# Kernel tuning notes

Hardware: AMD Instinct MI355X
Metric: run time of the kernel (lower is better)

## Reference

```python
import jax, jax.numpy as jnp
import numpy as np

N_NODES = 10000
W_DIM = 512
N_EDGES = 200000


def setup_inputs() -> dict:
    key = jax.random.key(0)
    k1, k2, k3 = jax.random.split(key, 3)
    z_drug = jax.random.normal(k1, (N_NODES, W_DIM), dtype=jnp.float32)
    # glorot-style init for the bilinear weight
    glorot_std = jnp.sqrt(2.0 / (W_DIM + W_DIM)).astype(jnp.float32)
    weight = jax.random.normal(k2, (W_DIM, W_DIM), dtype=jnp.float32) * glorot_std
    batch_edges = jax.random.randint(k3, (2, N_EDGES), 0, N_NODES, dtype=jnp.int64)
    return {"z_drug": z_drug, "weight": weight, "batch_edges": batch_edges}


def reference(z_drug, weight, batch_edges):
    # edge_type == 'drug_drug': both endpoints come from the drug table.
    row_embed = z_drug[batch_edges[0]]  # [E, d]
    col_embed = z_drug[batch_edges[1]]  # [E, d]
    # score_e = row_e @ W @ col_e  == diag((Z1 W) Z2^T) without the N x N blowup
    score = jnp.einsum('ed,df,ef->e', row_embed, weight, col_embed)
    return jax.nn.sigmoid(score)  # is_sigmoid=True default
```

## Files before the change

kernel.cpp:

```cpp
#include <hip/hip_runtime.h>
#include <math.h>

#define DIM     512
#define NNODES  10000
#define NEDGES  200000
#define MPAD    10240
#define NMB     160
#define NGRP    5
#define NB      (NGRP * NNODES)
#define SCAN_N  49
#define GEMM_GRID (NMB * 4)

#define SCAT_BASE  49
#define SCAT_N     196
#define GEMM_BASE  245
#define FUSE_GRID  (GEMM_BASE + GEMM_GRID)

using floatx4 = __attribute__((ext_vector_type(4))) float;
using half8   = __attribute__((ext_vector_type(8))) _Float16;
using half2v  = __attribute__((ext_vector_type(2))) _Float16;
typedef unsigned long long ull;

template <int N> struct IC { static constexpr int v = N; };

__device__ inline float dot2acc(half2v a, half2v b, float c) {
#if __has_builtin(__builtin_amdgcn_fdot2)
    return __builtin_amdgcn_fdot2(a, b, c, false);
#else
    return fmaf((float)a[0], (float)b[0], fmaf((float)a[1], (float)b[1], c));
#endif
}

__device__ inline int aload(const int* p) {
    return __hip_atomic_load(p, __ATOMIC_RELAXED, __HIP_MEMORY_SCOPE_AGENT);
}
__device__ inline void astore(int* p, int v) {
    __hip_atomic_store(p, v, __ATOMIC_RELAXED, __HIP_MEMORY_SCOPE_AGENT);
}
__device__ inline void waitflag(int* f, int target) {
    while (__hip_atomic_load(f, __ATOMIC_RELAXED, __HIP_MEMORY_SCOPE_AGENT) < target)
        __builtin_amdgcn_s_sleep(8);
    __atomic_signal_fence(__ATOMIC_ACQUIRE);
}
__device__ inline void signal(int* f) {
    __atomic_signal_fence(__ATOMIC_RELEASE);
    __hip_atomic_fetch_add(f, 1, __ATOMIC_RELAXED, __HIP_MEMORY_SCOPE_AGENT);
}

#define PREP_ZBLK 2560
#define PREP_WBASE PREP_ZBLK
#define PREP_HBASE (PREP_ZBLK + 64)
#define PREP_HBLK  64
#define PREP_GRID  (PREP_HBASE + PREP_HBLK)
__global__ __launch_bounds__(256) void prep(const float* __restrict__ Z,
                                            const float* __restrict__ W,
                                            const int* __restrict__ eidx,
                                            _Float16* __restrict__ Zh16,
                                            _Float16* __restrict__ Wh16t,
                                            int* __restrict__ counts) {
    const int b = blockIdx.x;
    const int t = threadIdx.x;

    if (b < PREP_ZBLK) {
        const int idx8 = (b * 256 + t) * 8;
        const int m = idx8 >> 9;
        float x[8];
        if (m < NNODES) {
            float4 v0 = *(const float4*)(Z + idx8);
            float4 v1 = *(const float4*)(Z + idx8 + 4);
            x[0]=v0.x; x[1]=v0.y; x[2]=v0.z; x[3]=v0.w;
            x[4]=v1.x; x[5]=v1.y; x[6]=v1.z; x[7]=v1.w;
        } else {
            #pragma unroll
            for (int j = 0; j < 8; ++j) x[j] = 0.f;
        }
        half8 h;
        #pragma unroll
        for (int j = 0; j < 8; ++j) h[j] = (_Float16)x[j];
        *(half8*)(Zh16 + idx8) = h;
    } else if (b < PREP_HBASE) {
        __shared__ float tile[64][65];
        const int wb = b - PREP_WBASE;
        const int kb = (wb >> 3) * 64;
        const int nb = (wb & 7) * 64;
        const int kk = t >> 2;
        const int ch = t & 3;

        const float* src = W + (size_t)(kb + kk) * DIM + nb + ch * 16;
        #pragma unroll
        for (int q = 0; q < 4; ++q) {
            float4 v = *(const float4*)(src + q * 4);
            tile[kk][ch * 16 + q * 4 + 0] = v.x;
            tile[kk][ch * 16 + q * 4 + 1] = v.y;
            tile[kk][ch * 16 + q * 4 + 2] = v.z;
            tile[kk][ch * 16 + q * 4 + 3] = v.w;
        }
        __syncthreads();

        const int nn = kk;
        half8 h0, h1;
        #pragma unroll
        for (int i = 0; i < 8; ++i) h0[i] = (_Float16)tile[ch * 16 + i][nn];
        #pragma unroll
        for (int i = 0; i < 8; ++i) h1[i] = (_Float16)tile[ch * 16 + 8 + i][nn];
        _Float16* d = Wh16t + (size_t)(nb + nn) * DIM + kb + ch * 16;
        *(half8*)(d)     = h0;
        *(half8*)(d + 8) = h1;
    } else {
        const int hb = b - PREP_HBASE;
        for (int e = hb * 256 + t; e < NEDGES; e += PREP_HBLK * 256) {
            int r = eidx[e];
            int c = eidx[NEDGES + e];
            atomicAdd(&counts[(c >> 11) * NNODES + r], 1);
        }
    }
}

__global__ __launch_bounds__(256, 3) void gemm_sort(
        const _Float16* __restrict__ Zh16,
        const _Float16* __restrict__ Wh16t,
        _Float16* __restrict__ ZWh,
        const int* __restrict__ eidx,
        int* __restrict__ counts,
        int* __restrict__ cursor,
        int* __restrict__ blksum,
        ull* __restrict__ slots,
        int* __restrict__ flags)
{
    __shared__ _Float16 Abuf[2][2 * 64 * 32];
    __shared__ _Float16 Bbuf[2][2 * 128 * 32];
    __shared__ int wsum[4];
    __shared__ int sbase;

    const int t   = threadIdx.x;
    const int bid = blockIdx.x;

    if (bid >= GEMM_BASE) {
        const int s8  = bid - GEMM_BASE;
        const int cxd = bid & 7;
        const int rr  = s8 >> 3;
        const int mg  = (rr >> 2) * 8 + cxd;
        const int m0  = mg * 64;
        const int n0  = (rr & 3) * 128;

        const int l  = t & 63;
        const int w  = t >> 6;
        const int wn = w * 32;
        const int lm = l & 15;
        const int lq = l >> 4;
        const unsigned wbase = (unsigned)(t & 192);

        floatx4 acc[4][2] = {};

        auto stage = [&](int buf, int k0) {
            #pragma unroll
            for (int p = 0; p < 2; ++p) {
                const int s   = p * 256 + t;
                const int kk  = s >> 8;
                const int row = (s >> 2) & 63;
                const int ch  = s & 3;
                const _Float16* src = Zh16 + (size_t)(m0 + row) * DIM + k0 + kk * 32 + ch * 8;
                __builtin_amdgcn_global_load_lds(
                    (const __attribute__((address_space(1))) void*)src,
                    (__attribute__((address_space(3))) void*)&Abuf[buf][(p * 256 + wbase) * 8],
                    16, 0, 0);
            }
            #pragma unroll
            for (int p = 0; p < 4; ++p) {
                const int s   = p * 256 + t;
                const int kk  = s >> 9;
                const int row = (s >> 2) & 127;
                const int ch  = s & 3;
                const _Float16* src = Wh16t + (size_t)(n0 + row) * DIM + k0 + kk * 32 + ch * 8;
                __builtin_amdgcn_global_load_lds(
                    (const __attribute__((address_space(1))) void*)src,
                    (__attribute__((address_space(3))) void*)&Bbuf[buf][(p * 256 + wbase) * 8],
                    16, 0, 0);
            }
        };

        stage(0, 0);
        stage(1, 64);

        auto step = [&](auto Sc) {
            constexpr int S   = decltype(Sc)::v;
            constexpr int buf = S & 1;
            if constexpr (S < 7) asm volatile("s_waitcnt vmcnt(6)" ::: "memory");
            else                 asm volatile("s_waitcnt vmcnt(0)" ::: "memory");
            __builtin_amdgcn_sched_barrier(0);
            __builtin_amdgcn_s_barrier();
            __builtin_amdgcn_sched_barrier(0);

            half8 aF[2][4], bF[2][2];
            #pragma unroll
            for (int kk = 0; kk < 2; ++kk) {
                #pragma unroll
                for (int i = 0; i < 4; ++i)
                    aF[kk][i] = *(const half8*)&Abuf[buf][kk * 2048 + (16 * i + lm) * 32 + lq * 8];
                #pragma unroll
                for (int j = 0; j < 2; ++j)
                    bF[kk][j] = *(const half8*)&Bbuf[buf][kk * 4096 + (wn + 16 * j + lm) * 32 + lq * 8];
            }
            asm volatile("s_waitcnt lgkmcnt(0)" ::: "memory");
            __builtin_amdgcn_sched_barrier(0);
            __builtin_amdgcn_s_barrier();
            __builtin_amdgcn_sched_barrier(0);

            if constexpr (S < 6) stage(buf, (S + 2) * 64);

            #pragma unroll
            for (int kk = 0; kk < 2; ++kk)
                #pragma unroll
                for (int i = 0; i < 4; ++i)
                    #pragma unroll
                    for (int j = 0; j < 2; ++j)
                        acc[i][j] = __builtin_amdgcn_mfma_f32_16x16x32_f16(
                            aF[kk][i], bF[kk][j], acc[i][j], 0, 0, 0);
        };

        step(IC<0>{}); step(IC<1>{}); step(IC<2>{}); step(IC<3>{});
        step(IC<4>{}); step(IC<5>{}); step(IC<6>{}); step(IC<7>{});

        #pragma unroll
        for (int i = 0; i < 4; ++i)
            #pragma unroll
            for (int j = 0; j < 2; ++j)
                #pragma unroll
                for (int r = 0; r < 4; ++r) {
                    const int gm = m0 + 16 * i + lq * 4 + r;
                    const int gn = n0 + wn + 16 * j + lm;
                    if (gm < NNODES)
                        ZWh[(size_t)gm * DIM + gn] = (_Float16)acc[i][j][r];
                }
        return;
    }

    if (bid < SCAT_BASE) {
        const int b = bid;
        const int lane = t & 63;
        const int wv   = t >> 6;

        const int base = b * 1024 + t * 4;
        int v0 = 0, v1 = 0, v2 = 0, v3 = 0;
        if (base + 3 < NB) {
            v0 = aload(counts + base);
            v1 = aload(counts + base + 1);
            v2 = aload(counts + base + 2);
            v3 = aload(counts + base + 3);
        } else {
            if (base     < NB) v0 = aload(counts + base);
            if (base + 1 < NB) v1 = aload(counts + base + 1);
            if (base + 2 < NB) v2 = aload(counts + base + 2);
        }
        const int ts = v0 + v1 + v2 + v3;
        int incl = ts;
        #pragma unroll
        for (int off = 1; off < 64; off <<= 1) {
            int u = __shfl_up(incl, off, 64);
            if (lane >= off) incl += u;
        }
        if (lane == 63) wsum[wv] = incl;
        __syncthreads();
        int wb = 0;
        #pragma unroll
        for (int k = 0; k < 4; ++k) if (k < wv) wb += wsum[k];
        const int ex   = wb + incl - ts;
        const int pre0 = ex;
        const int pre1 = ex + v0;
        const int pre2 = pre1 + v1;
        const int pre3 = pre2 + v2;
        if (t == 255) astore(blksum + b, wb + incl);
        __syncthreads();
        if (t == 0) { signal(&flags[1]); waitflag(&flags[1], SCAN_N); }
        __syncthreads();

        if (t < 64) {
            int v = (t < b) ? aload(blksum + t) : 0;
            #pragma unroll
            for (int off = 32; off > 0; off >>= 1)
                v += __shfl_xor(v, off, 64);
            if (t == 0) sbase = v;
        }
        __syncthreads();
        const int b0 = sbase;

        if (base + 3 < NB) {
            astore(cursor + base,     b0 + pre0);
            astore(cursor + base + 1, b0 + pre1);
            astore(cursor + base + 2, b0 + pre2);
            astore(cursor + base + 3, b0 + pre3);
        } else {
            if (base     < NB) astore(cursor + base,     b0 + pre0);
            if (base + 1 < NB) astore(cursor + base + 1, b0 + pre1);
            if (base + 2 < NB) astore(cursor + base + 2, b0 + pre2);
        }
        __syncthreads();
        if (t == 0) signal(&flags[2]);
        return;
    }

    {
        if (t == 0) waitflag(&flags[2], SCAN_N);
        __syncthreads();

        for (int e = (bid - SCAT_BASE) * 256 + t; e < NEDGES; e += SCAT_N * 256) {
            int r = eidx[e];
            int c = eidx[NEDGES + e];
            int pos = atomicAdd(&cursor[(c >> 11) * NNODES + r], 1);
            slots[pos] = (ull)(((unsigned)c << 18) | (unsigned)e) | ((ull)(unsigned)r << 32);
        }
    }
}

__global__ __launch_bounds__(256) void edge_score_f(const _Float16* __restrict__ ZWh,
                                                    const _Float16* __restrict__ Zh,
                                                    const ull* __restrict__ slots,
                                                    float* __restrict__ out) {
    const int t    = threadIdx.x;
    const int wgid = blockIdx.x * 4 + (t >> 6);
    const int lane = t & 63;
    const int gq   = lane >> 4;
    const int sl   = lane & 15;

    const int ii = wgid * 4 + gq;
    const ull  v = slots[ii];
    const unsigned k = (unsigned)v;
    const int c = (int)(k >> 18);
    const int r = (int)((v >> 32) & 0xFFFFu);

    const _Float16* rp = ZWh + (size_t)r * DIM + sl * 32;
    const _Float16* cp = Zh  + (size_t)c * DIM + sl * 32;

    half8 ra0 = *(const half8*)(rp);
    half8 ra1 = *(const half8*)(rp + 8);
    half8 ra2 = *(const half8*)(rp + 16);
    half8 ra3 = *(const half8*)(rp + 24);
    half8 c0  = *(const half8*)(cp);
    half8 c1  = *(const half8*)(cp + 8);
    half8 c2  = *(const half8*)(cp + 16);
    half8 c3  = *(const half8*)(cp + 24);

    float s = 0.f;
    #pragma unroll
    for (int d = 0; d < 4; ++d) {
        s = dot2acc((half2v){ra0[2*d], ra0[2*d+1]}, (half2v){c0[2*d], c0[2*d+1]}, s);
        s = dot2acc((half2v){ra1[2*d], ra1[2*d+1]}, (half2v){c1[2*d], c1[2*d+1]}, s);
        s = dot2acc((half2v){ra2[2*d], ra2[2*d+1]}, (half2v){c2[2*d], c2[2*d+1]}, s);
        s = dot2acc((half2v){ra3[2*d], ra3[2*d+1]}, (half2v){c3[2*d], c3[2*d+1]}, s);
    }

    s += __shfl_xor(s, 1, 64);
    s += __shfl_xor(s, 2, 64);
    s += __shfl_xor(s, 4, 64);
    s += __shfl_xor(s, 8, 64);

    if (sl == 0)
        out[k & 0x3FFFFu] = 1.0f / (1.0f + expf(-s));
}

#define GTM 128
#define GTN 64
#define GTK 16
#define LDA 132
#define LDB 68

__global__ __launch_bounds__(256) void gemm_zw(const float* __restrict__ A,
                                               const float* __restrict__ B,
                                               float* __restrict__ C) {
    __shared__ float As[GTK * LDA];
    __shared__ float Bs[GTK * LDB];

    const int t  = threadIdx.x;
    const int m0 = blockIdx.x * GTM;
    const int n0 = blockIdx.y * GTN;
    const int tx = t & 15;
    const int ty = t >> 4;

    float acc[8][4] = {};

    for (int k0 = 0; k0 < DIM; k0 += GTK) {
        #pragma unroll
        for (int p = 0; p < 2; ++p) {
            int f  = t + p * 256;
            int mm = f >> 2;
            int kq = f & 3;
            int m  = m0 + mm;
            float4 v = make_float4(0.f, 0.f, 0.f, 0.f);
            if (m < NNODES)
                v = *(const float4*)(A + (size_t)m * DIM + k0 + kq * 4);
            As[(kq * 4 + 0) * LDA + mm] = v.x;
            As[(kq * 4 + 1) * LDA + mm] = v.y;
            As[(kq * 4 + 2) * LDA + mm] = v.z;
            As[(kq * 4 + 3) * LDA + mm] = v.w;
        }
        {
            int kb = t >> 4, n4 = t & 15;
            *(float4*)&Bs[kb * LDB + n4 * 4] =
                *(const float4*)(B + (size_t)(k0 + kb) * DIM + n0 + n4 * 4);
        }
        __syncthreads();

        #pragma unroll
        for (int kk = 0; kk < GTK; ++kk) {
            float4 a0 = *(const float4*)&As[kk * LDA + ty * 8];
            float4 a1 = *(const float4*)&As[kk * LDA + ty * 8 + 4];
            float4 b  = *(const float4*)&Bs[kk * LDB + tx * 4];
            float av[8] = {a0.x, a0.y, a0.z, a0.w, a1.x, a1.y, a1.z, a1.w};
            float bv[4] = {b.x, b.y, b.z, b.w};
            #pragma unroll
            for (int i = 0; i < 8; ++i)
                #pragma unroll
                for (int j = 0; j < 4; ++j)
                    acc[i][j] = fmaf(av[i], bv[j], acc[i][j]);
        }
        __syncthreads();
    }

    #pragma unroll
    for (int i = 0; i < 8; ++i) {
        int m = m0 + ty * 8 + i;
        if (m < NNODES)
            *(float4*)(C + (size_t)m * DIM + n0 + tx * 4) =
                make_float4(acc[i][0], acc[i][1], acc[i][2], acc[i][3]);
    }
}

__global__ __launch_bounds__(256) void edge_score(const float* __restrict__ ZW,
                                                  const float* __restrict__ Z,
                                                  const int* __restrict__ eidx,
                                                  float* __restrict__ out) {
    const int e    = blockIdx.x * 4 + (threadIdx.x >> 6);
    const int lane = threadIdx.x & 63;

    const int r = eidx[e];
    const int c = eidx[NEDGES + e];

    const float4* pr = (const float4*)(ZW + (size_t)r * DIM);
    const float4* pc = (const float4*)(Z  + (size_t)c * DIM);

    float4 a0 = pr[lane * 2 + 0];
    float4 a1 = pr[lane * 2 + 1];
    float4 b0 = pc[lane * 2 + 0];
    float4 b1 = pc[lane * 2 + 1];

    float s = a0.x * b0.x;
    s = fmaf(a0.y, b0.y, s);
    s = fmaf(a0.z, b0.z, s);
    s = fmaf(a0.w, b0.w, s);
    s = fmaf(a1.x, b1.x, s);
    s = fmaf(a1.y, b1.y, s);
    s = fmaf(a1.z, b1.z, s);
    s = fmaf(a1.w, b1.w, s);

    #pragma unroll
    for (int off = 32; off > 0; off >>= 1)
        s += __shfl_xor(s, off, 64);

    if (lane == 0)
        out[e] = 1.0f / (1.0f + expf(-s));
}

extern "C" void kernel_launch(void* const* d_in, const int* in_sizes, int n_in,
                              void* d_out, int out_size, void* d_ws, size_t ws_size,
                              hipStream_t stream) {
    const float* Z  = (const float*)d_in[0];
    const float* W  = (const float*)d_in[1];
    const int*   EI = (const int*)d_in[2];
    float* out = (float*)d_out;

    char* p = (char*)d_ws;
    _Float16* ZWh   = (_Float16*)p;  p += (size_t)MPAD * DIM * 2;
    _Float16* Zh16  = (_Float16*)p;  p += (size_t)MPAD * DIM * 2;
    _Float16* Wh16t = (_Float16*)p;  p += (size_t)DIM * DIM * 2;
    int* counts  = (int*)p;          p += (size_t)NB * 4;
    int* flags   = (int*)p;          p += 4 * 4;
    int* cursor  = (int*)p;          p += (size_t)NB * 4;
    int* blksum  = (int*)p;          p += (size_t)SCAN_N * 4;
    ull* slots   = (ull*)p;          p += (size_t)NEDGES * 8;
    const size_t need_full = (size_t)(p - (char*)d_ws);

    if (ws_size >= need_full) {
        hipMemsetAsync(counts, 0, (size_t)NB * 4 + 16, stream);
        prep<<<PREP_GRID, 256, 0, stream>>>(Z, W, EI, Zh16, Wh16t, counts);
        gemm_sort<<<FUSE_GRID, 256, 0, stream>>>(Zh16, Wh16t, ZWh, EI, counts,
                                                 cursor, blksum, slots, flags);
        edge_score_f<<<NEDGES / 16, 256, 0, stream>>>(ZWh, Zh16, slots, out);
    } else {
        float* ZW = (float*)d_ws;
        dim3 g1((NNODES + GTM - 1) / GTM, DIM / GTN);
        gemm_zw<<<g1, 256, 0, stream>>>(Z, W, ZW);
        edge_score<<<NEDGES / 4, 256, 0, stream>>>(ZW, Z, EI, out);
    }
}
```

Measured before the change: 139.8 us.

## Drop edge counting-sort and score edges in original order

Removes the histogram, scan and scatter stages that bucketed edges by (column group, row) for gather locality, along with the memset and the cross-block flag spinning. The edge scoring kernel now reads endpoint indices straight from the edge list and writes outputs in edge order. This saves the atomics, the extra kernel work and the slot array traffic, but gives up the cache locality of the sorted gathers of ZW and Z rows.

Result: faster. 128.8 us, median of 2 (-7.8%).

```diff
diff --git a/kernel.cpp b/kernel.cpp
--- a/kernel.cpp
+++ b/kernel.cpp
@@ -6,20 +6,11 @@
 #define NEDGES  200000
 #define MPAD    10240
 #define NMB     160
-#define NGRP    5
-#define NB      (NGRP * NNODES)
-#define SCAN_N  49
 #define GEMM_GRID (NMB * 4)
-
-#define SCAT_BASE  49
-#define SCAT_N     196
-#define GEMM_BASE  245
-#define FUSE_GRID  (GEMM_BASE + GEMM_GRID)
 
 using floatx4 = __attribute__((ext_vector_type(4))) float;
 using half8   = __attribute__((ext_vector_type(8))) _Float16;
 using half2v  = __attribute__((ext_vector_type(2))) _Float16;
-typedef unsigned long long ull;
 
 template <int N> struct IC { static constexpr int v = N; };
 
@@ -31,33 +22,12 @@
 #endif
 }
 
-__device__ inline int aload(const int* p) {
-    return __hip_atomic_load(p, __ATOMIC_RELAXED, __HIP_MEMORY_SCOPE_AGENT);
-}
-__device__ inline void astore(int* p, int v) {
-    __hip_atomic_store(p, v, __ATOMIC_RELAXED, __HIP_MEMORY_SCOPE_AGENT);
-}
-__device__ inline void waitflag(int* f, int target) {
-    while (__hip_atomic_load(f, __ATOMIC_RELAXED, __HIP_MEMORY_SCOPE_AGENT) < target)
-        __builtin_amdgcn_s_sleep(8);
-    __atomic_signal_fence(__ATOMIC_ACQUIRE);
-}
-__device__ inline void signal(int* f) {
-    __atomic_signal_fence(__ATOMIC_RELEASE);
-    __hip_atomic_fetch_add(f, 1, __ATOMIC_RELAXED, __HIP_MEMORY_SCOPE_AGENT);
-}
-
 #define PREP_ZBLK 2560
-#define PREP_WBASE PREP_ZBLK
-#define PREP_HBASE (PREP_ZBLK + 64)
-#define PREP_HBLK  64
-#define PREP_GRID  (PREP_HBASE + PREP_HBLK)
+#define PREP_GRID (PREP_ZBLK + 64)
 __global__ __launch_bounds__(256) void prep(const float* __restrict__ Z,
                                             const float* __restrict__ W,
-                                            const int* __restrict__ eidx,
                                             _Float16* __restrict__ Zh16,
-                                            _Float16* __restrict__ Wh16t,
-                                            int* __restrict__ counts) {
+                                            _Float16* __restrict__ Wh16t) {
     const int b = blockIdx.x;
     const int t = threadIdx.x;
 
@@ -78,9 +48,9 @@
         #pragma unroll
         for (int j = 0; j < 8; ++j) h[j] = (_Float16)x[j];
         *(half8*)(Zh16 + idx8) = h;
-    } else if (b < PREP_HBASE) {
+    } else {
         __shared__ float tile[64][65];
-        const int wb = b - PREP_WBASE;
+        const int wb = b - PREP_ZBLK;
         const int kb = (wb >> 3) * 64;
         const int nb = (wb & 7) * 64;
         const int kk = t >> 2;
@@ -106,227 +76,129 @@
         _Float16* d = Wh16t + (size_t)(nb + nn) * DIM + kb + ch * 16;
         *(half8*)(d)     = h0;
         *(half8*)(d + 8) = h1;
-    } else {
-        const int hb = b - PREP_HBASE;
-        for (int e = hb * 256 + t; e < NEDGES; e += PREP_HBLK * 256) {
-            int r = eidx[e];
-            int c = eidx[NEDGES + e];
-            atomicAdd(&counts[(c >> 11) * NNODES + r], 1);
-        }
-    }
-}
-
-__global__ __launch_bounds__(256, 3) void gemm_sort(
+    }
+}
+
+__global__ __launch_bounds__(256, 3) void gemm_f16(
         const _Float16* __restrict__ Zh16,
         const _Float16* __restrict__ Wh16t,
-        _Float16* __restrict__ ZWh,
-        const int* __restrict__ eidx,
-        int* __restrict__ counts,
-        int* __restrict__ cursor,
-        int* __restrict__ blksum,
-        ull* __restrict__ slots,
-        int* __restrict__ flags)
+        _Float16* __restrict__ ZWh)
 {
     __shared__ _Float16 Abuf[2][2 * 64 * 32];
     __shared__ _Float16 Bbuf[2][2 * 128 * 32];
-    __shared__ int wsum[4];
-    __shared__ int sbase;
 
     const int t   = threadIdx.x;
     const int bid = blockIdx.x;
 
-    if (bid >= GEMM_BASE) {
-        const int s8  = bid - GEMM_BASE;
-        const int cxd = bid & 7;
-        const int rr  = s8 >> 3;
-        const int mg  = (rr >> 2) * 8 + cxd;
-        const int m0  = mg * 64;
-        const int n0  = (rr & 3) * 128;
-
-        const int l  = t & 63;
-        const int w  = t >> 6;
-        const int wn = w * 32;
-        const int lm = l & 15;
-        const int lq = l >> 4;
-        const unsigned wbase = (unsigned)(t & 192);
-
-        floatx4 acc[4][2] = {};
-
-        auto stage = [&](int buf, int k0) {
-            #pragma unroll
-            for (int p = 0; p < 2; ++p) {
-                const int s   = p * 256 + t;
-                const int kk  = s >> 8;
-                const int row = (s >> 2) & 63;
-                const int ch  = s & 3;
-                const _Float16* src = Zh16 + (size_t)(m0 + row) * DIM + k0 + kk * 32 + ch * 8;
-                __builtin_amdgcn_global_load_lds(
-                    (const __attribute__((address_space(1))) void*)src,
-                    (__attribute__((address_space(3))) void*)&Abuf[buf][(p * 256 + wbase) * 8],
-                    16, 0, 0);
-            }
-            #pragma unroll
-            for (int p = 0; p < 4; ++p) {
-                const int s   = p * 256 + t;
-                const int kk  = s >> 9;
-                const int row = (s >> 2) & 127;
-                const int ch  = s & 3;
-                const _Float16* src = Wh16t + (size_t)(n0 + row) * DIM + k0 + kk * 32 + ch * 8;
-                __builtin_amdgcn_global_load_lds(
-                    (const __attribute__((address_space(1))) void*)src,
-                    (__attribute__((address_space(3))) void*)&Bbuf[buf][(p * 256 + wbase) * 8],
-                    16, 0, 0);
-            }
-        };
-
-        stage(0, 0);
-        stage(1, 64);
-
-        auto step = [&](auto Sc) {
-            constexpr int S   = decltype(Sc)::v;
-            constexpr int buf = S & 1;
-            if constexpr (S < 7) asm volatile("s_waitcnt vmcnt(6)" ::: "memory");
-            else                 asm volatile("s_waitcnt vmcnt(0)" ::: "memory");
-            __builtin_amdgcn_sched_barrier(0);
-            __builtin_amdgcn_s_barrier();
-            __builtin_amdgcn_sched_barrier(0);
-
-            half8 aF[2][4], bF[2][2];
-            #pragma unroll
-            for (int kk = 0; kk < 2; ++kk) {
-                #pragma unroll
-                for (int i = 0; i < 4; ++i)
-                    aF[kk][i] = *(const half8*)&Abuf[buf][kk * 2048 + (16 * i + lm) * 32 + lq * 8];
+    const int cxd = bid & 7;
+    const int rr  = bid >> 3;
+    const int mg  = (rr >> 2) * 8 + cxd;
+    const int m0  = mg * 64;
+    const int n0  = (rr & 3) * 128;
+
+    const int l  = t & 63;
+    const int w  = t >> 6;
+    const int wn = w * 32;
+    const int lm = l & 15;
+    const int lq = l >> 4;
+    const unsigned wbase = (unsigned)(t & 192);
+
+    floatx4 acc[4][2] = {};
+
+    auto stage = [&](int buf, int k0) {
+        #pragma unroll
+        for (int p = 0; p < 2; ++p) {
+            const int s   = p * 256 + t;
+            const int kk  = s >> 8;
+            const int row = (s >> 2) & 63;
+            const int ch  = s & 3;
+            const _Float16* src = Zh16 + (size_t)(m0 + row) * DIM + k0 + kk * 32 + ch * 8;
+            __builtin_amdgcn_global_load_lds(
+                (const __attribute__((address_space(1))) void*)src,
+                (__attribute__((address_space(3))) void*)&Abuf[buf][(p * 256 + wbase) * 8],
+                16, 0, 0);
+        }
+        #pragma unroll
+        for (int p = 0; p < 4; ++p) {
+            const int s   = p * 256 + t;
+            const int kk  = s >> 9;
+            const int row = (s >> 2) & 127;
+            const int ch  = s & 3;
+            const _Float16* src = Wh16t + (size_t)(n0 + row) * DIM + k0 + kk * 32 + ch * 8;
+            __builtin_amdgcn_global_load_lds(
+                (const __attribute__((address_space(1))) void*)src,
+                (__attribute__((address_space(3))) void*)&Bbuf[buf][(p * 256 + wbase) * 8],
+                16, 0, 0);
+        }
+    };
+
+    stage(0, 0);
+    stage(1, 64);
+
+    auto step = [&](auto Sc) {
+        constexpr int S   = decltype(Sc)::v;
+        constexpr int buf = S & 1;
+        if constexpr (S < 7) asm volatile("s_waitcnt vmcnt(6)" ::: "memory");
+        else                 asm volatile("s_waitcnt vmcnt(0)" ::: "memory");
+        __builtin_amdgcn_sched_barrier(0);
+        __builtin_amdgcn_s_barrier();
+        __builtin_amdgcn_sched_barrier(0);
+
+        half8 aF[2][4], bF[2][2];
+        #pragma unroll
+        for (int kk = 0; kk < 2; ++kk) {
+            #pragma unroll
+            for (int i = 0; i < 4; ++i)
+                aF[kk][i] = *(const half8*)&Abuf[buf][kk * 2048 + (16 * i + lm) * 32 + lq * 8];
+            #pragma unroll
+            for (int j = 0; j < 2; ++j)
+                bF[kk][j] = *(const half8*)&Bbuf[buf][kk * 4096 + (wn + 16 * j + lm) * 32 + lq * 8];
+        }
+        asm volatile("s_waitcnt lgkmcnt(0)" ::: "memory");
+        __builtin_amdgcn_sched_barrier(0);
+        __builtin_amdgcn_s_barrier();
+        __builtin_amdgcn_sched_barrier(0);
+
+        if constexpr (S < 6) stage(buf, (S + 2) * 64);
+
+        #pragma unroll
+        for (int kk = 0; kk < 2; ++kk)
+            #pragma unroll
+            for (int i = 0; i < 4; ++i)
                 #pragma unroll
                 for (int j = 0; j < 2; ++j)
-                    bF[kk][j] = *(const half8*)&Bbuf[buf][kk * 4096 + (wn + 16 * j + lm) * 32 + lq * 8];
+                    acc[i][j] = __builtin_amdgcn_mfma_f32_16x16x32_f16(
+                        aF[kk][i], bF[kk][j], acc[i][j], 0, 0, 0);
+    };
+
+    step(IC<0>{}); step(IC<1>{}); step(IC<2>{}); step(IC<3>{});
+    step(IC<4>{}); step(IC<5>{}); step(IC<6>{}); step(IC<7>{});
+
+    #pragma unroll
+    for (int i = 0; i < 4; ++i)
+        #pragma unroll
+        for (int j = 0; j < 2; ++j)
+            #pragma unroll
+            for (int r = 0; r < 4; ++r) {
+                const int gm = m0 + 16 * i + lq * 4 + r;
+                const int gn = n0 + wn + 16 * j + lm;
+                if (gm < NNODES)
+                    ZWh[(size_t)gm * DIM + gn] = (_Float16)acc[i][j][r];
             }
-            asm volatile("s_waitcnt lgkmcnt(0)" ::: "memory");
-            __builtin_amdgcn_sched_barrier(0);
-            __builtin_amdgcn_s_barrier();
-            __builtin_amdgcn_sched_barrier(0);
-
-            if constexpr (S < 6) stage(buf, (S + 2) * 64);
-
-            #pragma unroll
-            for (int kk = 0; kk < 2; ++kk)
-                #pragma unroll
-                for (int i = 0; i < 4; ++i)
-                    #pragma unroll
-                    for (int j = 0; j < 2; ++j)
-                        acc[i][j] = __builtin_amdgcn_mfma_f32_16x16x32_f16(
-                            aF[kk][i], bF[kk][j], acc[i][j], 0, 0, 0);
-        };
-
-        step(IC<0>{}); step(IC<1>{}); step(IC<2>{}); step(IC<3>{});
-        step(IC<4>{}); step(IC<5>{}); step(IC<6>{}); step(IC<7>{});
-
-        #pragma unroll
-        for (int i = 0; i < 4; ++i)
-            #pragma unroll
-            for (int j = 0; j < 2; ++j)
-                #pragma unroll
-                for (int r = 0; r < 4; ++r) {
-                    const int gm = m0 + 16 * i + lq * 4 + r;
-                    const int gn = n0 + wn + 16 * j + lm;
-                    if (gm < NNODES)
-                        ZWh[(size_t)gm * DIM + gn] = (_Float16)acc[i][j][r];
-                }
-        return;
-    }
-
-    if (bid < SCAT_BASE) {
-        const int b = bid;
-        const int lane = t & 63;
-        const int wv   = t >> 6;
-
-        const int base = b * 1024 + t * 4;
-        int v0 = 0, v1 = 0, v2 = 0, v3 = 0;
-        if (base + 3 < NB) {
-            v0 = aload(counts + base);
-            v1 = aload(counts + base + 1);
-            v2 = aload(counts + base + 2);
-            v3 = aload(counts + base + 3);
-        } else {
-            if (base     < NB) v0 = aload(counts + base);
-            if (base + 1 < NB) v1 = aload(counts + base + 1);
-            if (base + 2 < NB) v2 = aload(counts + base + 2);
-        }
-        const int ts = v0 + v1 + v2 + v3;
-        int incl = ts;
-        #pragma unroll
-        for (int off = 1; off < 64; off <<= 1) {
-            int u = __shfl_up(incl, off, 64);
-            if (lane >= off) incl += u;
-        }
-        if (lane == 63) wsum[wv] = incl;
-        __syncthreads();
-        int wb = 0;
-        #pragma unroll
-        for (int k = 0; k < 4; ++k) if (k < wv) wb += wsum[k];
-        const int ex   = wb + incl - ts;
-        const int pre0 = ex;
-        const int pre1 = ex + v0;
-        const int pre2 = pre1 + v1;
-        const int pre3 = pre2 + v2;
-        if (t == 255) astore(blksum + b, wb + incl);
-        __syncthreads();
-        if (t == 0) { signal(&flags[1]); waitflag(&flags[1], SCAN_N); }
-        __syncthreads();
-
-        if (t < 64) {
-            int v = (t < b) ? aload(blksum + t) : 0;
-            #pragma unroll
-            for (int off = 32; off > 0; off >>= 1)
-                v += __shfl_xor(v, off, 64);
-            if (t == 0) sbase = v;
-        }
-        __syncthreads();
-        const int b0 = sbase;
-
-        if (base + 3 < NB) {
-            astore(cursor + base,     b0 + pre0);
-            astore(cursor + base + 1, b0 + pre1);
-            astore(cursor + base + 2, b0 + pre2);
-            astore(cursor + base + 3, b0 + pre3);
-        } else {
-            if (base     < NB) astore(cursor + base,     b0 + pre0);
-            if (base + 1 < NB) astore(cursor + base + 1, b0 + pre1);
-            if (base + 2 < NB) astore(cursor + base + 2, b0 + pre2);
-        }
-        __syncthreads();
-        if (t == 0) signal(&flags[2]);
-        return;
-    }
-
-    {
-        if (t == 0) waitflag(&flags[2], SCAN_N);
-        __syncthreads();
-
-        for (int e = (bid - SCAT_BASE) * 256 + t; e < NEDGES; e += SCAT_N * 256) {
-            int r = eidx[e];
-            int c = eidx[NEDGES + e];
-            int pos = atomicAdd(&cursor[(c >> 11) * NNODES + r], 1);
-            slots[pos] = (ull)(((unsigned)c << 18) | (unsigned)e) | ((ull)(unsigned)r << 32);
-        }
-    }
-}
-
-__global__ __launch_bounds__(256) void edge_score_f(const _Float16* __restrict__ ZWh,
+}
+
+__global__ __launch_bounds__(256) void edge_score_u(const _Float16* __restrict__ ZWh,
                                                     const _Float16* __restrict__ Zh,
-                                                    const ull* __restrict__ slots,
+                                                    const int* __restrict__ eidx,
                                                     float* __restrict__ out) {
     const int t    = threadIdx.x;
-    const int wgid = blockIdx.x * 4 + (t >> 6);
     const int lane = t & 63;
     const int gq   = lane >> 4;
     const int sl   = lane & 15;
 
-    const int ii = wgid * 4 + gq;
-    const ull  v = slots[ii];
-    const unsigned k = (unsigned)v;
-    const int c = (int)(k >> 18);
-    const int r = (int)((v >> 32) & 0xFFFFu);
+    const int e = blockIdx.x * 16 + (t >> 6) * 4 + gq;
+    const int r = eidx[e];
+    const int c = eidx[NEDGES + e];
 
     const _Float16* rp = ZWh + (size_t)r * DIM + sl * 32;
     const _Float16* cp = Zh  + (size_t)c * DIM + sl * 32;
@@ -355,7 +227,7 @@
     s += __shfl_xor(s, 8, 64);
 
     if (sl == 0)
-        out[k & 0x3FFFFu] = 1.0f / (1.0f + expf(-s));
+        out[e] = 1.0f / (1.0f + expf(-s));
 }
 
 #define GTM 128
@@ -472,19 +344,12 @@
     _Float16* ZWh   = (_Float16*)p;  p += (size_t)MPAD * DIM * 2;
     _Float16* Zh16  = (_Float16*)p;  p += (size_t)MPAD * DIM * 2;
     _Float16* Wh16t = (_Float16*)p;  p += (size_t)DIM * DIM * 2;
-    int* counts  = (int*)p;          p += (size_t)NB * 4;
-    int* flags   = (int*)p;          p += 4 * 4;
-    int* cursor  = (int*)p;          p += (size_t)NB * 4;
-    int* blksum  = (int*)p;          p += (size_t)SCAN_N * 4;
-    ull* slots   = (ull*)p;          p += (size_t)NEDGES * 8;
     const size_t need_full = (size_t)(p - (char*)d_ws);
 
     if (ws_size >= need_full) {
-        hipMemsetAsync(counts, 0, (size_t)NB * 4 + 16, stream);
-        prep<<<PREP_GRID, 256, 0, stream>>>(Z, W, EI, Zh16, Wh16t, counts);
-        gemm_sort<<<FUSE_GRID, 256, 0, stream>>>(Zh16, Wh16t, ZWh, EI, counts,
-                                                 cursor, blksum, slots, flags);
-        edge_score_f<<<NEDGES / 16, 256, 0, stream>>>(ZWh, Zh16, slots, out);
+        prep<<<PREP_GRID, 256, 0, stream>>>(Z, W, Zh16, Wh16t);
+        gemm_f16<<<GEMM_GRID, 256, 0, stream>>>(Zh16, Wh16t, ZWh);
+        edge_score_u<<<NEDGES / 16, 256, 0, stream>>>(ZWh, Zh16, EI, out);
     } else {
         float* ZW = (float*)d_ws;
         dim3 g1((NNODES + GTM - 1) / GTM, DIM / GTN);
```
